# Performance work log

Measured on AMD Instinct MI355X. Metric: run time of the kernel, lower is better.

The kernel has to match this reference:

```python
import jax, jax.numpy as jnp
import numpy as np

B = 4096
N_FEAT = 4
VOCAB = 100000
EMB = 64
N_NEG = 3
TEMP = 1.0
EPS = 1e-8  # torch.cosine_similarity eps


def setup_inputs() -> dict:
    key = jax.random.key(0)
    ks = jax.random.split(key, 12)
    inp = {}
    inp['user_ids'] = jax.random.randint(ks[0], (B, N_FEAT), 0, VOCAB)
    inp['item_ids'] = jax.random.randint(ks[1], (B, N_FEAT), 0, VOCAB)
    inp['sw_ids'] = jax.random.randint(ks[2], (B,), 0, VOCAB)
    inp['user_tables'] = jax.random.normal(ks[3], (N_FEAT, VOCAB, EMB), jnp.float32) * 0.05
    inp['item_tables'] = jax.random.normal(ks[4], (N_FEAT, VOCAB, EMB), jnp.float32) * 0.05
    # sample weights must be positive (log is taken)
    inp['sw_table'] = jax.random.uniform(ks[5], (VOCAB,), jnp.float32) * 0.99 + 0.01
    inp['uW1'] = jax.random.normal(ks[6], (256, 256), jnp.float32) * 0.05
    inp['ub1'] = jnp.zeros((256,), jnp.float32)
    inp['uW2'] = jax.random.normal(ks[7], (256, 128), jnp.float32) * 0.05
    inp['ub2'] = jnp.zeros((128,), jnp.float32)
    inp['iW1'] = jax.random.normal(ks[8], (256, 256), jnp.float32) * 0.05
    inp['ib1'] = jnp.zeros((256,), jnp.float32)
    inp['iW2'] = jax.random.normal(ks[9], (256, 128), jnp.float32) * 0.05
    inp['ib2'] = jnp.zeros((128,), jnp.float32)
    return inp


def _embed(tables, ids):
    # tables: [F, V, E], ids: [B, F] -> [B, F*E]
    e = jax.vmap(lambda tbl, idx: tbl[idx], in_axes=(0, 1))(tables, ids)  # [F, B, E]
    return jnp.transpose(e, (1, 0, 2)).reshape(ids.shape[0], -1)


def _mlp(x, W1, b1, W2, b2):
    # torch-rechub MLP with output_layer=False: activation after every layer
    h = jax.nn.relu(x @ W1 + b1)
    return jax.nn.relu(h @ W2 + b2)


def reference(user_ids, item_ids, sw_ids, user_tables, item_tables, sw_table,
              uW1, ub1, uW2, ub2, iW1, ib1, iW2, ib2):
    u = _mlp(_embed(user_tables, user_ids), uW1, ub1, uW2, ub2)   # [B, 128]
    v = _mlp(_embed(item_tables, item_ids), iW1, ib1, iW2, ib2)   # [B, 128]
    un = u / jnp.maximum(jnp.linalg.norm(u, axis=-1, keepdims=True), EPS)
    vn = v / jnp.maximum(jnp.linalg.norm(v, axis=-1, keepdims=True), EPS)
    pred = un @ vn.T                                              # [B, B] cosine sim
    sw = sw_table[sw_ids]                                         # [B]
    scores = pred - jnp.log(sw)[None, :]                          # debias per item column
    # in-batch negative sampling: row i pairs with cols (i..i+n_neg) mod B
    rows = jnp.repeat(jnp.arange(B), N_NEG + 1)
    cols = ((jnp.arange(B)[:, None] + jnp.arange(N_NEG + 1)[None, :]) % B).reshape(-1)
    out = scores[rows, cols] / TEMP
    return out.reshape(B, N_NEG + 1)
```

## Files before the change

kernel.cpp:

```cpp
#include <hip/hip_runtime.h>
#include <math.h>

#define BATCH 4096
#define NFEAT 4
#define VOCAB 100000
#define EMB 64
#define D_IN 256
#define D_H 256
#define D_O 128
#define XS_STRIDE 264
#define YS_STRIDE 132

typedef __attribute__((ext_vector_type(8))) short bf16x8;
typedef __attribute__((ext_vector_type(4))) float f32x4;

__device__ inline ushort f2bf(float f) {
  union { float f; unsigned u; } v; v.f = f;
  unsigned u = v.u;
  return (ushort)((u + 0x7fffu + ((u >> 16) & 1u)) >> 16);
}

__device__ inline bf16x8 load_wfrag(const float* __restrict__ wp, int strideN) {
  bf16x8 b;
#pragma unroll
  for (int j = 0; j < 8; j++) b[j] = (short)f2bf(wp[(size_t)j * strideN]);
  return b;
}

__global__ __launch_bounds__(512) void fused_kernel(
    const int* __restrict__ user_ids, const int* __restrict__ item_ids,
    const int* __restrict__ sw_ids,
    const float* __restrict__ user_tables, const float* __restrict__ item_tables,
    const float* __restrict__ sw_table,
    const float* __restrict__ uW1, const float* __restrict__ ub1,
    const float* __restrict__ uW2, const float* __restrict__ ub2,
    const float* __restrict__ iW1, const float* __restrict__ ib1,
    const float* __restrict__ iW2, const float* __restrict__ ib2,
    float* __restrict__ out) {
  const int r0 = blockIdx.x * 16;
  const int tid = threadIdx.x;
  const int lane = tid & 63;
  const int w = tid >> 6;

  __shared__ ushort Xs_u[16][XS_STRIDE];
  __shared__ ushort Xs_i[32][XS_STRIDE];
  __shared__ ushort Hs_u[16][XS_STRIDE];
  __shared__ ushort Hs_i[32][XS_STRIDE];
  __shared__ float Ys_u[16][YS_STRIDE];
  __shared__ float Ys_i[32][YS_STRIDE];

  for (int s = tid; s < 2240; s += 512) {
    bool isu = s < 1024;
    int t = isu ? s : s - 1024;
    int row = t >> 6;
    int c4 = t & 63;
    int f = c4 >> 4;
    int grow = (r0 + row) & (BATCH - 1);
    const int* ids = isu ? user_ids : item_ids;
    const float* tab = isu ? user_tables : item_tables;
    int id = ids[(size_t)grow * NFEAT + f];
    float4 v = ((const float4*)(tab + ((size_t)f * VOCAB + (size_t)id) * EMB))[c4 & 15];
    ushort4 o = {f2bf(v.x), f2bf(v.y), f2bf(v.z), f2bf(v.w)};
    if (isu) *(ushort4*)&Xs_u[row][c4 * 4] = o;
    else     *(ushort4*)&Xs_i[row][c4 * 4] = o;
  }
  for (int z = tid; z < 13 * 66; z += 512) {
    int row = 19 + z / 66, c = z % 66;
    ushort4 zz = {0, 0, 0, 0};
    *(ushort4*)&Xs_i[row][c * 4] = zz;
  }
  __syncthreads();

  const int m = lane & 15;
  const int quad = lane >> 4;

#pragma unroll
  for (int s = 0; s < 6; s++) {
    int t = w * 6 + s;
    int tile = t >> 4;
    int ct = t & 15;
    const ushort (*X)[XS_STRIDE] = tile == 0 ? Xs_u : (tile == 1 ? Xs_i : Xs_i + 16);
    ushort (*H)[XS_STRIDE] = tile == 0 ? Hs_u : (tile == 1 ? Hs_i : Hs_i + 16);
    const float* Wm = tile == 0 ? uW1 : iW1;
    const float* bm = tile == 0 ? ub1 : ib1;
    bf16x8 a[8];
#pragma unroll
    for (int k0 = 0; k0 < 8; k0++)
      a[k0] = *(const bf16x8*)&X[m][k0 * 32 + quad * 8];
    int n = ct * 16 + m;
    const float* wp = Wm + (size_t)(quad * 8) * D_H + n;
    f32x4 acc = {0.f, 0.f, 0.f, 0.f};
#pragma unroll
    for (int k0 = 0; k0 < 8; k0++)
      acc = __builtin_amdgcn_mfma_f32_16x16x32_bf16(
          a[k0], load_wfrag(wp + (size_t)k0 * 32 * D_H, D_H), acc, 0, 0, 0);
    float bias = bm[n];
#pragma unroll
    for (int reg = 0; reg < 4; reg++)
      H[quad * 4 + reg][n] = f2bf(fmaxf(acc[reg] + bias, 0.f));
  }
  __syncthreads();

#pragma unroll
  for (int s = 0; s < 3; s++) {
    int t = w * 3 + s;
    int tile = t >> 3;
    int ct = t & 7;
    const ushort (*H)[XS_STRIDE] = tile == 0 ? Hs_u : (tile == 1 ? Hs_i : Hs_i + 16);
    float (*Y)[YS_STRIDE] = tile == 0 ? Ys_u : (tile == 1 ? Ys_i : Ys_i + 16);
    const float* Wm = tile == 0 ? uW2 : iW2;
    const float* bm = tile == 0 ? ub2 : ib2;
    bf16x8 h[8];
#pragma unroll
    for (int k0 = 0; k0 < 8; k0++)
      h[k0] = *(const bf16x8*)&H[m][k0 * 32 + quad * 8];
    int n = ct * 16 + m;
    const float* wp = Wm + (size_t)(quad * 8) * D_O + n;
    f32x4 acc = {0.f, 0.f, 0.f, 0.f};
#pragma unroll
    for (int k0 = 0; k0 < 8; k0++)
      acc = __builtin_amdgcn_mfma_f32_16x16x32_bf16(
          h[k0], load_wfrag(wp + (size_t)k0 * 32 * D_O, D_O), acc, 0, 0, 0);
    float bias = bm[n];
#pragma unroll
    for (int reg = 0; reg < 4; reg++)
      Y[quad * 4 + reg][n] = fmaxf(acc[reg] + bias, 0.f);
  }
  __syncthreads();

#pragma unroll
  for (int rr = 0; rr < 5; rr++) {
    int row = rr * 8 + w;
    if (row < 35) {
      float* Y = row < 16 ? &Ys_u[row][0] : &Ys_i[row - 16][0];
      float y0 = Y[lane];
      float y1 = Y[64 + lane];
      float s2 = y0 * y0 + y1 * y1;
#pragma unroll
      for (int off = 32; off; off >>= 1) s2 += __shfl_xor(s2, off);
      float inv = 1.f / fmaxf(sqrtf(s2), 1e-8f);
      Y[lane] = y0 * inv;
      Y[64 + lane] = y1 * inv;
    }
  }
  __syncthreads();

#pragma unroll
  for (int rr = 0; rr < 2; rr++) {
    int il = w * 2 + rr;
    int i = r0 + il;
    float u0 = Ys_u[il][lane];
    float u1 = Ys_u[il][64 + lane];
#pragma unroll
    for (int j = 0; j < 4; j++) {
      int cl = il + j;
      float v0 = Ys_i[cl][lane];
      float v1 = Ys_i[cl][64 + lane];
      float d = u0 * v0 + u1 * v1;
#pragma unroll
      for (int off = 32; off; off >>= 1) d += __shfl_xor(d, off);
      if (lane == 0) {
        int c = (i + j) & (BATCH - 1);
        out[(size_t)i * 4 + j] = d - logf(sw_table[sw_ids[c]]);
      }
    }
  }
}

extern "C" void kernel_launch(void* const* d_in, const int* in_sizes, int n_in,
                              void* d_out, int out_size, void* d_ws, size_t ws_size,
                              hipStream_t stream) {
  (void)in_sizes; (void)n_in; (void)out_size; (void)d_ws; (void)ws_size;
  const int*   user_ids    = (const int*)d_in[0];
  const int*   item_ids    = (const int*)d_in[1];
  const int*   sw_ids      = (const int*)d_in[2];
  const float* user_tables = (const float*)d_in[3];
  const float* item_tables = (const float*)d_in[4];
  const float* sw_table    = (const float*)d_in[5];
  const float* uW1 = (const float*)d_in[6];
  const float* ub1 = (const float*)d_in[7];
  const float* uW2 = (const float*)d_in[8];
  const float* ub2 = (const float*)d_in[9];
  const float* iW1 = (const float*)d_in[10];
  const float* ib1 = (const float*)d_in[11];
  const float* iW2 = (const float*)d_in[12];
  const float* ib2 = (const float*)d_in[13];
  float* out = (float*)d_out;

  fused_kernel<<<BATCH / 16, 512, 0, stream>>>(
      user_ids, item_ids, sw_ids, user_tables, item_tables, sw_table,
      uW1, ub1, uW2, ub2, iW1, ib1, iW2, ib2, out);
}
```

Before: 226.0 us.

## Pre-transpose weights to bf16 in a prep kernel for vectorized MFMA B-fragment loads

Adds a prep kernel that converts the four MLP weight matrices to bf16 and transposes them to [N][K] in the workspace. The fused kernel then loads each MFMA B fragment with one 16-byte vector load instead of eight strided fp32 loads plus conversions. This cuts global memory traffic and per-fragment conversion work across all 256 blocks. The cost is an extra kernel launch that runs on every call.

```diff
diff --git a/kernel.cpp b/kernel.cpp
--- a/kernel.cpp
+++ b/kernel.cpp
@@ -20,11 +20,25 @@
   return (ushort)((u + 0x7fffu + ((u >> 16) & 1u)) >> 16);
 }
 
-__device__ inline bf16x8 load_wfrag(const float* __restrict__ wp, int strideN) {
-  bf16x8 b;
-#pragma unroll
-  for (int j = 0; j < 8; j++) b[j] = (short)f2bf(wp[(size_t)j * strideN]);
-  return b;
+__global__ __launch_bounds__(256) void prep_kernel(
+    const float* __restrict__ uW1, const float* __restrict__ uW2,
+    const float* __restrict__ iW1, const float* __restrict__ iW2,
+    ushort* __restrict__ W1tu, ushort* __restrict__ W2tu,
+    ushort* __restrict__ W1ti, ushort* __restrict__ W2ti) {
+  int idx = blockIdx.x * 256 + threadIdx.x;
+  if (idx < 65536) {
+    int n = idx >> 8, k = idx & 255;
+    W1tu[idx] = f2bf(uW1[k * 256 + n]);
+  } else if (idx < 131072) {
+    int j = idx - 65536; int n = j >> 8, k = j & 255;
+    W1ti[j] = f2bf(iW1[k * 256 + n]);
+  } else if (idx < 163840) {
+    int j = idx - 131072; int n = j >> 8, k = j & 255;
+    W2tu[j] = f2bf(uW2[k * 128 + n]);
+  } else {
+    int j = idx - 163840; int n = j >> 8, k = j & 255;
+    W2ti[j] = f2bf(iW2[k * 128 + n]);
+  }
 }
 
 __global__ __launch_bounds__(512) void fused_kernel(
@@ -32,10 +46,10 @@
     const int* __restrict__ sw_ids,
     const float* __restrict__ user_tables, const float* __restrict__ item_tables,
     const float* __restrict__ sw_table,
-    const float* __restrict__ uW1, const float* __restrict__ ub1,
-    const float* __restrict__ uW2, const float* __restrict__ ub2,
-    const float* __restrict__ iW1, const float* __restrict__ ib1,
-    const float* __restrict__ iW2, const float* __restrict__ ib2,
+    const ushort* __restrict__ W1tu, const float* __restrict__ ub1,
+    const ushort* __restrict__ W2tu, const float* __restrict__ ub2,
+    const ushort* __restrict__ W1ti, const float* __restrict__ ib1,
+    const ushort* __restrict__ W2ti, const float* __restrict__ ib2,
     float* __restrict__ out) {
   const int r0 = blockIdx.x * 16;
   const int tid = threadIdx.x;
@@ -81,19 +95,19 @@
     int ct = t & 15;
     const ushort (*X)[XS_STRIDE] = tile == 0 ? Xs_u : (tile == 1 ? Xs_i : Xs_i + 16);
     ushort (*H)[XS_STRIDE] = tile == 0 ? Hs_u : (tile == 1 ? Hs_i : Hs_i + 16);
-    const float* Wm = tile == 0 ? uW1 : iW1;
+    const ushort* Wt = tile == 0 ? W1tu : W1ti;
     const float* bm = tile == 0 ? ub1 : ib1;
     bf16x8 a[8];
 #pragma unroll
     for (int k0 = 0; k0 < 8; k0++)
       a[k0] = *(const bf16x8*)&X[m][k0 * 32 + quad * 8];
     int n = ct * 16 + m;
-    const float* wp = Wm + (size_t)(quad * 8) * D_H + n;
+    const ushort* wp = Wt + (size_t)n * 256 + quad * 8;
     f32x4 acc = {0.f, 0.f, 0.f, 0.f};
 #pragma unroll
     for (int k0 = 0; k0 < 8; k0++)
       acc = __builtin_amdgcn_mfma_f32_16x16x32_bf16(
-          a[k0], load_wfrag(wp + (size_t)k0 * 32 * D_H, D_H), acc, 0, 0, 0);
+          a[k0], *(const bf16x8*)(wp + k0 * 32), acc, 0, 0, 0);
     float bias = bm[n];
 #pragma unroll
     for (int reg = 0; reg < 4; reg++)
@@ -108,19 +122,19 @@
     int ct = t & 7;
     const ushort (*H)[XS_STRIDE] = tile == 0 ? Hs_u : (tile == 1 ? Hs_i : Hs_i + 16);
     float (*Y)[YS_STRIDE] = tile == 0 ? Ys_u : (tile == 1 ? Ys_i : Ys_i + 16);
-    const float* Wm = tile == 0 ? uW2 : iW2;
+    const ushort* Wt = tile == 0 ? W2tu : W2ti;
     const float* bm = tile == 0 ? ub2 : ib2;
     bf16x8 h[8];
 #pragma unroll
     for (int k0 = 0; k0 < 8; k0++)
       h[k0] = *(const bf16x8*)&H[m][k0 * 32 + quad * 8];
     int n = ct * 16 + m;
-    const float* wp = Wm + (size_t)(quad * 8) * D_O + n;
+    const ushort* wp = Wt + (size_t)n * 256 + quad * 8;
     f32x4 acc = {0.f, 0.f, 0.f, 0.f};
 #pragma unroll
     for (int k0 = 0; k0 < 8; k0++)
       acc = __builtin_amdgcn_mfma_f32_16x16x32_bf16(
-          h[k0], load_wfrag(wp + (size_t)k0 * 32 * D_O, D_O), acc, 0, 0, 0);
+          h[k0], *(const bf16x8*)(wp + k0 * 32), acc, 0, 0, 0);
     float bias = bm[n];
 #pragma unroll
     for (int reg = 0; reg < 4; reg++)
@@ -170,7 +184,7 @@
 extern "C" void kernel_launch(void* const* d_in, const int* in_sizes, int n_in,
                               void* d_out, int out_size, void* d_ws, size_t ws_size,
                               hipStream_t stream) {
-  (void)in_sizes; (void)n_in; (void)out_size; (void)d_ws; (void)ws_size;
+  (void)in_sizes; (void)n_in; (void)out_size; (void)ws_size;
   const int*   user_ids    = (const int*)d_in[0];
   const int*   item_ids    = (const int*)d_in[1];
   const int*   sw_ids      = (const int*)d_in[2];
@@ -187,7 +201,14 @@
   const float* ib2 = (const float*)d_in[13];
   float* out = (float*)d_out;
 
+  ushort* W1tu = (ushort*)d_ws;
+  ushort* W1ti = W1tu + 256 * 256;
+  ushort* W2tu = W1ti + 256 * 256;
+  ushort* W2ti = W2tu + 128 * 256;
+
+  prep_kernel<<<768, 256, 0, stream>>>(uW1, uW2, iW1, iW2, W1tu, W2tu, W1ti, W2ti);
+
   fused_kernel<<<BATCH / 16, 512, 0, stream>>>(
       user_ids, item_ids, sw_ids, user_tables, item_tables, sw_table,
-      uW1, ub1, uW2, ub2, iW1, ib1, iW2, ib2, out);
-}
+      W1tu, ub1, W2tu, ub2, W1ti, ib1, W2ti, ib2, out);
+}
```

After: 223.9 us. No clear change (-0.9%).
